# Performance work log

Measured on AMD Instinct MI355X. Metric: run time of the kernel, lower is better.

## Reference

```python
import jax, jax.numpy as jnp
import numpy as np

NUM_NODES = 50000
NUM_GRAPHS = 64
HIDDEN = 256
F_IN = 256
NUM_EDGES = 800000


def setup_inputs() -> dict:
    key = jax.random.key(0)
    ks = jax.random.split(key, 8)
    x = jax.random.normal(ks[0], (NUM_NODES, F_IN), dtype=jnp.float32)
    edge_index = jax.random.randint(ks[1], (2, NUM_EDGES), 0, NUM_NODES, dtype=jnp.int64)
    batch = jnp.sort(jax.random.randint(ks[2], (NUM_NODES,), 0, NUM_GRAPHS, dtype=jnp.int64))
    # Glorot-ish init for weights, zeros for biases (as PyG GCNConv / Linear defaults)
    s1 = 1.0 / np.sqrt(F_IN)
    s2 = 1.0 / np.sqrt(HIDDEN)
    W1 = jax.random.uniform(ks[3], (F_IN, HIDDEN), jnp.float32, -s1, s1)
    b1 = jnp.zeros((HIDDEN,), jnp.float32)
    W2 = jax.random.uniform(ks[4], (HIDDEN, HIDDEN), jnp.float32, -s2, s2)
    b2 = jnp.zeros((HIDDEN,), jnp.float32)
    W_out = jax.random.uniform(ks[5], (HIDDEN, 1), jnp.float32, -s2, s2)
    b_out = jnp.zeros((1,), jnp.float32)
    return {"x": x, "edge_index": edge_index, "batch": batch,
            "W1": W1, "b1": b1, "W2": W2, "b2": b2,
            "W_out": W_out, "b_out": b_out}


def gcn_conv(x, W, b, src, dst, num_nodes):
    """GCNConv with added self-loops and symmetric D^{-1/2} A D^{-1/2} norm."""
    # degrees over edges incl. self-loops (src/dst already include them)
    deg = jax.ops.segment_sum(jnp.ones_like(src, dtype=x.dtype), dst,
                              num_segments=num_nodes)
    dinv = jax.lax.rsqrt(jnp.maximum(deg, 1e-12))
    norm = dinv[src] * dinv[dst]                       # [E+N]
    h = x @ W                                           # [N, H] dense GEMM
    msg = h[src] * norm[:, None]                        # gather + scale
    out = jax.ops.segment_sum(msg, dst, num_segments=num_nodes)  # scatter-add
    return out + b


def reference(x, edge_index, batch, W1, b1, W2, b2, W_out, b_out):
    n = x.shape[0]
    loops = jnp.arange(n, dtype=edge_index.dtype)
    src = jnp.concatenate([edge_index[0], loops])
    dst = jnp.concatenate([edge_index[1], loops])
    h = jax.nn.relu(gcn_conv(x, W1, b1, src, dst, n))
    h = jax.nn.relu(gcn_conv(h, W2, b2, src, dst, n))
    pooled = jax.ops.segment_sum(h, batch, num_segments=NUM_GRAPHS)  # [G, H]
    return pooled @ W_out + b_out
```

## Files before the change

### kernel.cpp

```cpp
#include <hip/hip_runtime.h>
#include <hip/hip_fp16.h>

#define N_NODES 50000
#define NFEAT   256
#define NGRAPH  64
#define NEDGE   800000
#define NBUCK   98
#define BWIN    16384

typedef __attribute__((ext_vector_type(8))) _Float16 half8;
typedef __attribute__((ext_vector_type(2))) _Float16 h2v;
typedef __attribute__((ext_vector_type(4))) float f32x4;
struct alignas(8) US4 { unsigned short x, y, z, w; };

static __device__ __forceinline__ float h2f(unsigned short u) {
    return __half2float(__ushort_as_half(u));
}
static __device__ __forceinline__ unsigned short f2h(float f) {
    return __half_as_ushort(__float2half(f));
}

__global__ void k_prep_w(const float* __restrict__ W1, const float* __restrict__ W2,
                         unsigned short* __restrict__ w1t, unsigned short* __restrict__ w2t,
                         int* __restrict__ bcnt, float* __restrict__ pooled) {
    const int l = blockIdx.x >> 8;
    const int idx = (blockIdx.x & 255) * 256 + threadIdx.x;
    const int n = idx >> 8, k = idx & 255;
    const float* W = l ? W2 : W1;
    unsigned short* wt = l ? w2t : w1t;
    wt[n * 256 + k] = f2h(W[k * 256 + n]);
    if (l == 0) {
        if (blockIdx.x == 0 && threadIdx.x < NBUCK) bcnt[threadIdx.x] = 0;
        if (blockIdx.x >= 1 && blockIdx.x <= 64) {
            const int p = (blockIdx.x - 1) * 256 + threadIdx.x;
            if (p < NGRAPH * NFEAT) pooled[p] = 0.f;
        }
    }
}

__global__ __launch_bounds__(256) void k_bin(const int* __restrict__ src,
                                             const int* __restrict__ dst,
                                             int* __restrict__ bcnt,
                                             unsigned int* __restrict__ tmp) {
    __shared__ int hist[NBUCK];
    __shared__ int base[NBUCK];
    const int t = threadIdx.x;
    if (t < NBUCK) hist[t] = 0;
    __syncthreads();
    const int e0 = blockIdx.x * 1024 + t * 4;
    int s[4], d[4], b[4], rk[4];
#pragma unroll
    for (int i = 0; i < 4; ++i) {
        const int e = e0 + i;
        if (e < NEDGE) {
            s[i] = src[e];
            d[i] = dst[e];
            b[i] = d[i] >> 9;
            rk[i] = atomicAdd(&hist[b[i]], 1);
        } else {
            b[i] = -1;
        }
    }
    __syncthreads();
    if (t < NBUCK) base[t] = atomicAdd(&bcnt[t], hist[t]);
    __syncthreads();
#pragma unroll
    for (int i = 0; i < 4; ++i) {
        if (b[i] >= 0)
            tmp[(size_t)b[i] * BWIN + base[b[i]] + rk[i]] =
                ((unsigned int)s[i] << 16) | (unsigned int)d[i];
    }
}

__global__ __launch_bounds__(256) void k_build(const unsigned int* __restrict__ tmp,
                                               const int* __restrict__ bcnt,
                                               int* __restrict__ row_start,
                                               float* __restrict__ dinv,
                                               unsigned short* __restrict__ csr) {
    __shared__ int cnt[512];
    __shared__ int cur[512];
    __shared__ int wtot[4];
    __shared__ int s_gb;
    const int bk = blockIdx.x, t = threadIdx.x;
    const int node0 = bk << 9;
    const int n = bcnt[bk];
    const unsigned int* rec = tmp + (size_t)bk * BWIN;
    cnt[t] = 0;
    cnt[t + 256] = 0;
    if (t < 64) {
        int part = 0;
        for (int i = t; i < bk; i += 64) part += bcnt[i];
#pragma unroll
        for (int off = 32; off; off >>= 1) part += __shfl_down(part, off, 64);
        if (t == 0) s_gb = part;
    }
    __syncthreads();
    for (int i = t; i < n; i += 256) atomicAdd(&cnt[rec[i] & 511], 1);
    __syncthreads();
    const int lane = t & 63, w = t >> 6;
    const int v0 = cnt[2 * t], v1 = cnt[2 * t + 1];
    const int ps = v0 + v1;
    int incl = ps;
#pragma unroll
    for (int off = 1; off < 64; off <<= 1) {
        int u = __shfl_up(incl, off, 64);
        if (lane >= off) incl += u;
    }
    if (lane == 63) wtot[w] = incl;
    __syncthreads();
    int wbase = 0;
#pragma unroll
    for (int k = 0; k < 4; ++k) wbase += (k < w) ? wtot[k] : 0;
    const int excl = wbase + incl - ps;
    const int gb = s_gb;
    const int g0 = node0 + 2 * t;
    if (g0 < N_NODES) {
        row_start[g0] = gb + excl;
        dinv[g0] = rsqrtf((float)v0 + 1.0f);
    }
    if (g0 + 1 < N_NODES) {
        row_start[g0 + 1] = gb + excl + v0;
        dinv[g0 + 1] = rsqrtf((float)v1 + 1.0f);
    }
    cur[2 * t] = gb + excl;
    cur[2 * t + 1] = gb + excl + v0;
    __syncthreads();
    for (int i = t; i < n; i += 256) {
        const unsigned int r = rec[i];
        const int pos = atomicAdd(&cur[r & 511], 1);
        csr[pos] = (unsigned short)(r >> 16);
    }
    if (bk == 0 && t == 0) row_start[N_NODES] = NEDGE;
}

template <bool AF32>
__global__ __launch_bounds__(256) void k_gemm_mfma(const float* __restrict__ Af,
                                                   const unsigned short* __restrict__ Ah,
                                                   const unsigned short* __restrict__ Wt,
                                                   const float* __restrict__ dinv,
                                                   unsigned short* __restrict__ Ch, int M) {
    __shared__ unsigned short lds[32768];
    const int t = threadIdx.x;
    const int m0 = blockIdx.x * 128;
    const int w = t >> 6, lane = t & 63;
    const int lr = lane & 15, g = lane >> 4;

    int boff[8];
#pragma unroll
    for (int ni = 0; ni < 8; ++ni) {
        const int n = ni * 16 + lr;
        boff[ni] = n * 32 + ((g ^ ((n >> 1) & 3)) << 3);
    }

    const int rbase = m0 + w * 32;
    half8 aA[8], aB[8];

#define STAGE(H)                                                                         \
    {                                                                                    \
        const unsigned short* wbase = Wt + (size_t)(H) * 128 * 256;                      \
        _Pragma("unroll") for (int it = 0; it < 16; ++it) {                              \
            const int unit = it * 256 + t;                                               \
            const int n = unit >> 5;                                                     \
            const int rem = unit & 31;                                                   \
            const int ks = rem >> 2, kg = rem & 3;                                       \
            const half8 v = *(const half8*)&wbase[n * 256 + rem * 8];                    \
            const int kgx = kg ^ ((n >> 1) & 3);                                         \
            *(half8*)&lds[ks * 4096 + n * 32 + kgx * 8] = v;                             \
        }                                                                                \
    }

#define LOADCHUNK(C, DST)                                                                \
    {                                                                                    \
        const int row = min(rbase + (C) * 16 + lr, M - 1);                               \
        _Pragma("unroll") for (int ks = 0; ks < 8; ++ks) {                               \
            if (AF32) {                                                                  \
                const float* ap = Af + (size_t)row * 256 + ks * 32 + g * 8;              \
                const float4 p0 = *(const float4*)ap;                                    \
                const float4 p1 = *(const float4*)(ap + 4);                              \
                half8 h;                                                                 \
                h[0] = (_Float16)p0.x; h[1] = (_Float16)p0.y;                            \
                h[2] = (_Float16)p0.z; h[3] = (_Float16)p0.w;                            \
                h[4] = (_Float16)p1.x; h[5] = (_Float16)p1.y;                            \
                h[6] = (_Float16)p1.z; h[7] = (_Float16)p1.w;                            \
                DST[ks] = h;                                                             \
            } else {                                                                     \
                DST[ks] = *(const half8*)(Ah + (size_t)(ks >> 2) * (size_t)N_NODES * 128 \
                                          + (size_t)row * 128 + (ks & 3) * 32 + g * 8);  \
            }                                                                            \
        }                                                                                \
    }

#define COMPUTE(C, SRC, H)                                                               \
    {                                                                                    \
        unsigned short* Chh = Ch + (size_t)(H) * (size_t)N_NODES * 128;                  \
        f32x4 acc[8] = {};                                                               \
        half8 bc[8];                                                                     \
        _Pragma("unroll") for (int ni = 0; ni < 8; ++ni)                                 \
            bc[ni] = *(const half8*)&lds[boff[ni]];                                      \
        _Pragma("unroll") for (int ks = 0; ks < 8; ++ks) {                               \
            half8 bn[8];                                                                 \
            if (ks < 7) {                                                                \
                _Pragma("unroll") for (int ni = 0; ni < 8; ++ni)                         \
                    bn[ni] = *(const half8*)&lds[(ks + 1) * 4096 + boff[ni]];            \
            }                                                                            \
            _Pragma("unroll") for (int ni = 0; ni < 8; ++ni)                             \
                acc[ni] = __builtin_amdgcn_mfma_f32_16x16x32_f16(bc[ni], SRC[ks],        \
                                                                 acc[ni], 0, 0, 0);      \
            _Pragma("unroll") for (int ni = 0; ni < 8; ++ni) bc[ni] = bn[ni];            \
        }                                                                                \
        const int row = rbase + (C) * 16 + lr;                                           \
        const float dv = dinv[min(row, M - 1)];                                          \
        if (row < M) {                                                                   \
            _Pragma("unroll") for (int ni = 0; ni < 8; ++ni) {                           \
                US4 o;                                                                   \
                o.x = f2h(acc[ni][0] * dv); o.y = f2h(acc[ni][1] * dv);                  \
                o.z = f2h(acc[ni][2] * dv); o.w = f2h(acc[ni][3] * dv);                  \
                *(US4*)(Chh + (size_t)row * 128 + ni * 16 + g * 4) = o;                  \
            }                                                                            \
        }                                                                                \
    }

    STAGE(0)
    __syncthreads();
    LOADCHUNK(0, aA)
    LOADCHUNK(1, aB)
    COMPUTE(0, aA, 0)
    COMPUTE(1, aB, 0)
    __syncthreads();
    STAGE(1)
    __syncthreads();
    COMPUTE(0, aA, 1)
    COMPUTE(1, aB, 1)

#undef STAGE
#undef LOADCHUNK
#undef COMPUTE
}

__global__ __launch_bounds__(256) void k_aggregate(const unsigned short* __restrict__ hs,
                                                   const int* __restrict__ row_start,
                                                   const unsigned short* __restrict__ csr,
                                                   const float* __restrict__ dinv,
                                                   const float* __restrict__ bias,
                                                   unsigned short* __restrict__ out) {
    const int wid = blockIdx.x * 4 + (threadIdx.x >> 6);
    if (wid >= 2 * N_NODES) return;
    const int half = (wid >= N_NODES) ? 1 : 0;
    const int node = wid - half * N_NODES;
    const int lane = threadIdx.x & 63;
    const int sub = lane >> 4;
    const int fl = lane & 15;
    const unsigned int* hu = (const unsigned int*)(hs + (size_t)half * N_NODES * 128);
    const h2v e0v = {(_Float16)1.0f, (_Float16)0.0f};
    const h2v e1v = {(_Float16)0.0f, (_Float16)1.0f};

    float acc[8] = {};
    const int s0 = row_start[node], s1 = row_start[node + 1];
    const unsigned short* row = csr + s0;
    const int n = s1 - s0;

#define EDGEPAIR(VA, VB)                                                                   \
    {                                                                                      \
        h2v s;                                                                             \
        s = __builtin_bit_cast(h2v, VA.x) + __builtin_bit_cast(h2v, VB.x);                 \
        acc[0] = __builtin_amdgcn_fdot2(s, e0v, acc[0], false);                            \
        acc[1] = __builtin_amdgcn_fdot2(s, e1v, acc[1], false);                            \
        s = __builtin_bit_cast(h2v, VA.y) + __builtin_bit_cast(h2v, VB.y);                 \
        acc[2] = __builtin_amdgcn_fdot2(s, e0v, acc[2], false);                            \
        acc[3] = __builtin_amdgcn_fdot2(s, e1v, acc[3], false);                            \
        s = __builtin_bit_cast(h2v, VA.z) + __builtin_bit_cast(h2v, VB.z);                 \
        acc[4] = __builtin_amdgcn_fdot2(s, e0v, acc[4], false);                            \
        acc[5] = __builtin_amdgcn_fdot2(s, e1v, acc[5], false);                            \
        s = __builtin_bit_cast(h2v, VA.w) + __builtin_bit_cast(h2v, VB.w);                 \
        acc[6] = __builtin_amdgcn_fdot2(s, e0v, acc[6], false);                            \
        acc[7] = __builtin_amdgcn_fdot2(s, e1v, acc[7], false);                            \
    }

    const int nfull = n & ~7;
    int j = 0;
    for (; j < nfull; j += 8) {
        const int sa = row[j + sub * 2];
        const int sb = row[j + sub * 2 + 1];
        const uint4 va = *(const uint4*)(hu + (size_t)sa * 64 + fl * 4);
        const uint4 vb = *(const uint4*)(hu + (size_t)sb * 64 + fl * 4);
        EDGEPAIR(va, vb)
    }
    if (j < n) {
        const int ia = j + sub * 2, ib = ia + 1;
        uint4 va = {0, 0, 0, 0}, vb = {0, 0, 0, 0};
        if (ia < n) va = *(const uint4*)(hu + (size_t)row[ia] * 64 + fl * 4);
        if (ib < n) vb = *(const uint4*)(hu + (size_t)row[ib] * 64 + fl * 4);
        EDGEPAIR(va, vb)
    }
#undef EDGEPAIR

#pragma unroll
    for (int i = 0; i < 8; ++i) {
        acc[i] += __shfl_xor(acc[i], 16, 64);
        acc[i] += __shfl_xor(acc[i], 32, 64);
    }

    if (sub == 0) {
        const float dd = dinv[node];
        const uint4 sh = *(const uint4*)(hu + (size_t)node * 64 + fl * 4);
        const float4 b0 = *(const float4*)(bias + half * 128 + fl * 8);
        const float4 b1 = *(const float4*)(bias + half * 128 + fl * 8 + 4);
        float r[8];
        r[0] = fmaf(acc[0] + h2f((unsigned short)(sh.x & 0xffff)), dd, b0.x);
        r[1] = fmaf(acc[1] + h2f((unsigned short)(sh.x >> 16)),    dd, b0.y);
        r[2] = fmaf(acc[2] + h2f((unsigned short)(sh.y & 0xffff)), dd, b0.z);
        r[3] = fmaf(acc[3] + h2f((unsigned short)(sh.y >> 16)),    dd, b0.w);
        r[4] = fmaf(acc[4] + h2f((unsigned short)(sh.z & 0xffff)), dd, b1.x);
        r[5] = fmaf(acc[5] + h2f((unsigned short)(sh.z >> 16)),    dd, b1.y);
        r[6] = fmaf(acc[6] + h2f((unsigned short)(sh.w & 0xffff)), dd, b1.z);
        r[7] = fmaf(acc[7] + h2f((unsigned short)(sh.w >> 16)),    dd, b1.w);
#pragma unroll
        for (int i = 0; i < 8; ++i) r[i] = fmaxf(r[i], 0.f);
        uint4 o;
        o.x = (unsigned int)f2h(r[0]) | ((unsigned int)f2h(r[1]) << 16);
        o.y = (unsigned int)f2h(r[2]) | ((unsigned int)f2h(r[3]) << 16);
        o.z = (unsigned int)f2h(r[4]) | ((unsigned int)f2h(r[5]) << 16);
        o.w = (unsigned int)f2h(r[6]) | ((unsigned int)f2h(r[7]) << 16);
        *(uint4*)((unsigned int*)(out + (size_t)half * N_NODES * 128) +
                  (size_t)node * 64 + fl * 4) = o;
    }
}

__global__ void k_pool(const unsigned short* __restrict__ h2, const int* __restrict__ batch,
                       float* __restrict__ pooled) {
    const int strip = blockIdx.x * 2 + (threadIdx.x >> 7);
    const int tf = threadIdx.x & 127;
    const int f = tf * 2;
    const unsigned short* base = h2 + (size_t)(f >> 7) * N_NODES * 128 + (f & 127);
    const int n0 = strip * 40, n1 = n0 + 40;
    int g = batch[n0];
    float ax = 0.f, ay = 0.f;
    for (int n = n0; n < n1; ++n) {
        const int bg = batch[n];
        if (bg != g) {
            unsafeAtomicAdd(&pooled[g * NFEAT + f], ax);
            unsafeAtomicAdd(&pooled[g * NFEAT + f + 1], ay);
            ax = ay = 0.f;
            g = bg;
        }
        const unsigned int u = *(const unsigned int*)(base + (size_t)n * 128);
        ax += h2f((unsigned short)(u & 0xffff));
        ay += h2f((unsigned short)(u >> 16));
    }
    unsafeAtomicAdd(&pooled[g * NFEAT + f], ax);
    unsafeAtomicAdd(&pooled[g * NFEAT + f + 1], ay);
}

__global__ void k_final(const float* __restrict__ pooled, const float* __restrict__ Wout,
                        const float* __restrict__ bout, float* __restrict__ out) {
    const int g = blockIdx.x, t = threadIdx.x;
    float v = pooled[g * NFEAT + t] * Wout[t];
#pragma unroll
    for (int off = 32; off > 0; off >>= 1) v += __shfl_down(v, off, 64);
    __shared__ float sred[4];
    if ((t & 63) == 0) sred[t >> 6] = v;
    __syncthreads();
    if (t == 0) out[g] = sred[0] + sred[1] + sred[2] + sred[3] + bout[0];
}

extern "C" void kernel_launch(void* const* d_in, const int* in_sizes, int n_in,
                              void* d_out, int out_size, void* d_ws, size_t ws_size,
                              hipStream_t stream) {
    const float* x     = (const float*)d_in[0];
    const int*   ei    = (const int*)d_in[1];
    const int*   batch = (const int*)d_in[2];
    const float* W1    = (const float*)d_in[3];
    const float* b1    = (const float*)d_in[4];
    const float* W2    = (const float*)d_in[5];
    const float* b2    = (const float*)d_in[6];
    const float* Wout  = (const float*)d_in[7];
    const float* bout  = (const float*)d_in[8];
    float* out = (float*)d_out;

    const int* srcp = ei;
    const int* dstp = ei + NEDGE;

    const size_t NE128 = (size_t)N_NODES * 128;
    unsigned short* hA = (unsigned short*)d_ws;
    unsigned short* hB = hA + 2 * NE128;
    float* dinv      = (float*)(hB + 2 * NE128);
    float* pooled    = dinv + N_NODES;
    int*   row_start = (int*)(pooled + NGRAPH * NFEAT);
    int*   bcnt      = row_start + N_NODES + 3;
    unsigned short* csr = (unsigned short*)(bcnt + NBUCK + 2);
    unsigned int* tmp = (unsigned int*)(csr + NEDGE);
    unsigned short* w1t = (unsigned short*)(tmp + (size_t)NBUCK * BWIN);
    unsigned short* w2t = w1t + 65536;

    k_prep_w<<<512, 256, 0, stream>>>(W1, W2, w1t, w2t, bcnt, pooled);

    k_bin<<<(NEDGE + 1023) / 1024, 256, 0, stream>>>(srcp, dstp, bcnt, tmp);
    k_build<<<NBUCK, 256, 0, stream>>>(tmp, bcnt, row_start, dinv, csr);

    const int ggrid = 391;
    const int agg_grid = (2 * N_NODES + 3) / 4;

    k_gemm_mfma<true><<<ggrid, 256, 0, stream>>>(x, nullptr, w1t, dinv, hA, N_NODES);
    k_aggregate<<<agg_grid, 256, 0, stream>>>(hA, row_start, csr, dinv, b1, hB);

    k_gemm_mfma<false><<<ggrid, 256, 0, stream>>>(nullptr, hB, w2t, dinv, hA, N_NODES);
    k_aggregate<<<agg_grid, 256, 0, stream>>>(hA, row_start, csr, dinv, b2, hB);

    k_pool<<<625, 256, 0, stream>>>(hB, batch, pooled);
    k_final<<<NGRAPH, 256, 0, stream>>>(pooled, Wout, bout, out);
}
```

Before: 252.3 us.

## Split aggregation into 128-byte feature quarters with interleaved block slices

The aggregation kernel now gives each wave a quarter of a node's features (64 halfs, one 128-byte line) instead of a half. Each 8-lane group handles one edge, so a wave processes 16 edges per iteration and uses an extra shuffle stage in the reduction. Block indices are interleaved so that consecutive blocks work on different feature quarters and node halves of the same node range, which is meant to improve cache locality and memory-level parallelism in the gather. The cost is twice as many waves, each re-reading the CSR row, plus one more cross-lane reduction step.

```diff
diff --git a/kernel.cpp b/kernel.cpp
--- a/kernel.cpp
+++ b/kernel.cpp
@@ -243,14 +243,18 @@
                                                    const float* __restrict__ dinv,
                                                    const float* __restrict__ bias,
                                                    unsigned short* __restrict__ out) {
-    const int wid = blockIdx.x * 4 + (threadIdx.x >> 6);
-    if (wid >= 2 * N_NODES) return;
-    const int half = (wid >= N_NODES) ? 1 : 0;
-    const int node = wid - half * N_NODES;
+    const int slice = blockIdx.x & 7;
+    const int nb = blockIdx.x >> 3;
+    const int line = slice >> 1;
+    const int nh = slice & 1;
+    const int half = line >> 1;
+    const int fq = line & 1;
+    const int node = nh * (N_NODES / 2) + nb * 4 + (threadIdx.x >> 6);
     const int lane = threadIdx.x & 63;
-    const int sub = lane >> 4;
-    const int fl = lane & 15;
-    const unsigned int* hu = (const unsigned int*)(hs + (size_t)half * N_NODES * 128);
+    const int slot = lane >> 3;
+    const int fl = lane & 7;
+    const unsigned int* hu =
+        (const unsigned int*)(hs + (size_t)half * N_NODES * 128) + fq * 32;
     const h2v e0v = {(_Float16)1.0f, (_Float16)0.0f};
     const h2v e1v = {(_Float16)0.0f, (_Float16)1.0f};
 
@@ -276,17 +280,17 @@
         acc[7] = __builtin_amdgcn_fdot2(s, e1v, acc[7], false);                            \
     }
 
-    const int nfull = n & ~7;
+    const int nfull = n & ~15;
     int j = 0;
-    for (; j < nfull; j += 8) {
-        const int sa = row[j + sub * 2];
-        const int sb = row[j + sub * 2 + 1];
+    for (; j < nfull; j += 16) {
+        const int sa = row[j + slot * 2];
+        const int sb = row[j + slot * 2 + 1];
         const uint4 va = *(const uint4*)(hu + (size_t)sa * 64 + fl * 4);
         const uint4 vb = *(const uint4*)(hu + (size_t)sb * 64 + fl * 4);
         EDGEPAIR(va, vb)
     }
     if (j < n) {
-        const int ia = j + sub * 2, ib = ia + 1;
+        const int ia = j + slot * 2, ib = ia + 1;
         uint4 va = {0, 0, 0, 0}, vb = {0, 0, 0, 0};
         if (ia < n) va = *(const uint4*)(hu + (size_t)row[ia] * 64 + fl * 4);
         if (ib < n) vb = *(const uint4*)(hu + (size_t)row[ib] * 64 + fl * 4);
@@ -296,15 +300,16 @@
 
 #pragma unroll
     for (int i = 0; i < 8; ++i) {
+        acc[i] += __shfl_xor(acc[i], 8, 64);
         acc[i] += __shfl_xor(acc[i], 16, 64);
         acc[i] += __shfl_xor(acc[i], 32, 64);
     }
 
-    if (sub == 0) {
+    if (slot == 0) {
         const float dd = dinv[node];
         const uint4 sh = *(const uint4*)(hu + (size_t)node * 64 + fl * 4);
-        const float4 b0 = *(const float4*)(bias + half * 128 + fl * 8);
-        const float4 b1 = *(const float4*)(bias + half * 128 + fl * 8 + 4);
+        const float4 b0 = *(const float4*)(bias + half * 128 + fq * 64 + fl * 8);
+        const float4 b1 = *(const float4*)(bias + half * 128 + fq * 64 + fl * 8 + 4);
         float r[8];
         r[0] = fmaf(acc[0] + h2f((unsigned short)(sh.x & 0xffff)), dd, b0.x);
         r[1] = fmaf(acc[1] + h2f((unsigned short)(sh.x >> 16)),    dd, b0.y);
@@ -322,7 +327,7 @@
         o.z = (unsigned int)f2h(r[4]) | ((unsigned int)f2h(r[5]) << 16);
         o.w = (unsigned int)f2h(r[6]) | ((unsigned int)f2h(r[7]) << 16);
         *(uint4*)((unsigned int*)(out + (size_t)half * N_NODES * 128) +
-                  (size_t)node * 64 + fl * 4) = o;
+                  (size_t)node * 64 + fq * 32 + fl * 4) = o;
     }
 }
 
@@ -398,7 +403,7 @@
     k_build<<<NBUCK, 256, 0, stream>>>(tmp, bcnt, row_start, dinv, csr);
 
     const int ggrid = 391;
-    const int agg_grid = (2 * N_NODES + 3) / 4;
+    const int agg_grid = (N_NODES / 2 / 4) * 8;
 
     k_gemm_mfma<true><<<ggrid, 256, 0, stream>>>(x, nullptr, w1t, dinv, hA, N_NODES);
     k_aggregate<<<agg_grid, 256, 0, stream>>>(hA, row_start, csr, dinv, b1, hB);
```

Measured after the change: 294.2 us. 1.17x slower.

## Fuse pooling with final projection and unroll aggregate gather loop by two

Applied to the files above, without the earlier changes.

Replaces the atomic-based pooling kernel and the separate final reduction with one kernel that binary-searches the sorted batch array for each graph's node range, sums features per graph and applies the output projection. This drops the pooled buffer, its zeroing and the float atomics. Only 64 blocks run, each walking about 780 nodes serially per column, so parallelism for that stage is low. Separately, the aggregate kernel's gather loop now processes 16 neighbours per iteration, putting more loads in flight.

```diff
diff --git a/kernel.cpp b/kernel.cpp
--- a/kernel.cpp
+++ b/kernel.cpp
@@ -22,20 +22,14 @@
 
 __global__ void k_prep_w(const float* __restrict__ W1, const float* __restrict__ W2,
                          unsigned short* __restrict__ w1t, unsigned short* __restrict__ w2t,
-                         int* __restrict__ bcnt, float* __restrict__ pooled) {
+                         int* __restrict__ bcnt) {
     const int l = blockIdx.x >> 8;
     const int idx = (blockIdx.x & 255) * 256 + threadIdx.x;
     const int n = idx >> 8, k = idx & 255;
     const float* W = l ? W2 : W1;
     unsigned short* wt = l ? w2t : w1t;
     wt[n * 256 + k] = f2h(W[k * 256 + n]);
-    if (l == 0) {
-        if (blockIdx.x == 0 && threadIdx.x < NBUCK) bcnt[threadIdx.x] = 0;
-        if (blockIdx.x >= 1 && blockIdx.x <= 64) {
-            const int p = (blockIdx.x - 1) * 256 + threadIdx.x;
-            if (p < NGRAPH * NFEAT) pooled[p] = 0.f;
-        }
-    }
+    if (l == 0 && blockIdx.x == 0 && threadIdx.x < NBUCK) bcnt[threadIdx.x] = 0;
 }
 
 __global__ __launch_bounds__(256) void k_bin(const int* __restrict__ src,
@@ -276,16 +270,21 @@
         acc[7] = __builtin_amdgcn_fdot2(s, e1v, acc[7], false);                            \
     }
 
-    const int nfull = n & ~7;
+    const int nfull = n & ~15;
     int j = 0;
-    for (; j < nfull; j += 8) {
-        const int sa = row[j + sub * 2];
-        const int sb = row[j + sub * 2 + 1];
-        const uint4 va = *(const uint4*)(hu + (size_t)sa * 64 + fl * 4);
-        const uint4 vb = *(const uint4*)(hu + (size_t)sb * 64 + fl * 4);
-        EDGEPAIR(va, vb)
-    }
-    if (j < n) {
+    for (; j < nfull; j += 16) {
+        const int a0 = row[j + sub * 2];
+        const int b0 = row[j + sub * 2 + 1];
+        const int a1 = row[j + 8 + sub * 2];
+        const int b1 = row[j + 8 + sub * 2 + 1];
+        const uint4 va0 = *(const uint4*)(hu + (size_t)a0 * 64 + fl * 4);
+        const uint4 vb0 = *(const uint4*)(hu + (size_t)b0 * 64 + fl * 4);
+        const uint4 va1 = *(const uint4*)(hu + (size_t)a1 * 64 + fl * 4);
+        const uint4 vb1 = *(const uint4*)(hu + (size_t)b1 * 64 + fl * 4);
+        EDGEPAIR(va0, vb0)
+        EDGEPAIR(va1, vb1)
+    }
+    for (; j < n; j += 8) {
         const int ia = j + sub * 2, ib = ia + 1;
         uint4 va = {0, 0, 0, 0}, vb = {0, 0, 0, 0};
         if (ia < n) va = *(const uint4*)(hu + (size_t)row[ia] * 64 + fl * 4);
@@ -326,37 +325,24 @@
     }
 }
 
-__global__ void k_pool(const unsigned short* __restrict__ h2, const int* __restrict__ batch,
-                       float* __restrict__ pooled) {
-    const int strip = blockIdx.x * 2 + (threadIdx.x >> 7);
-    const int tf = threadIdx.x & 127;
-    const int f = tf * 2;
-    const unsigned short* base = h2 + (size_t)(f >> 7) * N_NODES * 128 + (f & 127);
-    const int n0 = strip * 40, n1 = n0 + 40;
-    int g = batch[n0];
-    float ax = 0.f, ay = 0.f;
-    for (int n = n0; n < n1; ++n) {
-        const int bg = batch[n];
-        if (bg != g) {
-            unsafeAtomicAdd(&pooled[g * NFEAT + f], ax);
-            unsafeAtomicAdd(&pooled[g * NFEAT + f + 1], ay);
-            ax = ay = 0.f;
-            g = bg;
-        }
-        const unsigned int u = *(const unsigned int*)(base + (size_t)n * 128);
-        ax += h2f((unsigned short)(u & 0xffff));
-        ay += h2f((unsigned short)(u >> 16));
-    }
-    unsafeAtomicAdd(&pooled[g * NFEAT + f], ax);
-    unsafeAtomicAdd(&pooled[g * NFEAT + f + 1], ay);
-}
-
-__global__ void k_final(const float* __restrict__ pooled, const float* __restrict__ Wout,
-                        const float* __restrict__ bout, float* __restrict__ out) {
+__global__ __launch_bounds__(256) void k_pool_final(const unsigned short* __restrict__ hB,
+                                                    const int* __restrict__ batch,
+                                                    const float* __restrict__ Wout,
+                                                    const float* __restrict__ bout,
+                                                    float* __restrict__ out) {
     const int g = blockIdx.x, t = threadIdx.x;
-    float v = pooled[g * NFEAT + t] * Wout[t];
-#pragma unroll
-    for (int off = 32; off > 0; off >>= 1) v += __shfl_down(v, off, 64);
+    int lo = 0, hi = N_NODES;
+    while (lo < hi) { const int mid = (lo + hi) >> 1; if (batch[mid] < g) lo = mid + 1; else hi = mid; }
+    int lo2 = lo, hi2 = N_NODES;
+    while (lo2 < hi2) { const int mid = (lo2 + hi2) >> 1; if (batch[mid] < g + 1) lo2 = mid + 1; else hi2 = mid; }
+
+    const int half = t >> 7, c = t & 127;
+    const unsigned short* base = hB + (size_t)half * N_NODES * 128 + c;
+    float sum = 0.f;
+    for (int n = lo; n < lo2; ++n) sum += h2f(base[(size_t)n * 128]);
+    float v = sum * Wout[half * 128 + c];
+#pragma unroll
+    for (int off = 32; off; off >>= 1) v += __shfl_down(v, off, 64);
     __shared__ float sred[4];
     if ((t & 63) == 0) sred[t >> 6] = v;
     __syncthreads();
@@ -384,15 +370,14 @@
     unsigned short* hA = (unsigned short*)d_ws;
     unsigned short* hB = hA + 2 * NE128;
     float* dinv      = (float*)(hB + 2 * NE128);
-    float* pooled    = dinv + N_NODES;
-    int*   row_start = (int*)(pooled + NGRAPH * NFEAT);
+    int*   row_start = (int*)(dinv + N_NODES);
     int*   bcnt      = row_start + N_NODES + 3;
     unsigned short* csr = (unsigned short*)(bcnt + NBUCK + 2);
     unsigned int* tmp = (unsigned int*)(csr + NEDGE);
     unsigned short* w1t = (unsigned short*)(tmp + (size_t)NBUCK * BWIN);
     unsigned short* w2t = w1t + 65536;
 
-    k_prep_w<<<512, 256, 0, stream>>>(W1, W2, w1t, w2t, bcnt, pooled);
+    k_prep_w<<<512, 256, 0, stream>>>(W1, W2, w1t, w2t, bcnt);
 
     k_bin<<<(NEDGE + 1023) / 1024, 256, 0, stream>>>(srcp, dstp, bcnt, tmp);
     k_build<<<NBUCK, 256, 0, stream>>>(tmp, bcnt, row_start, dinv, csr);
@@ -406,6 +391,5 @@
     k_gemm_mfma<false><<<ggrid, 256, 0, stream>>>(nullptr, hB, w2t, dinv, hA, N_NODES);
     k_aggregate<<<agg_grid, 256, 0, stream>>>(hA, row_start, csr, dinv, b2, hB);
 
-    k_pool<<<625, 256, 0, stream>>>(hB, batch, pooled);
-    k_final<<<NGRAPH, 256, 0, stream>>>(pooled, Wout, bout, out);
-}
+    k_pool_final<<<NGRAPH, 256, 0, stream>>>(hB, batch, Wout, bout, out);
+}
```

New measurement: 460.3 us. +82.4%, slower.
